# Kernel tuning notes

Measured on AMD Instinct MI355X. Metric: run time of the kernel, lower is better.

## Reference

```python
import jax, jax.numpy as jnp
import numpy as np

B, N, FIN, FOUT, H, U = 2, 2048, 128, 128, 4, 1024
ALPHA = 0.2  # LeakyReLU negative slope
NEG = -9e15  # mask value from the original code


def setup_inputs() -> dict:
    key = jax.random.key(0)
    k0, k1, k2, k3, k4 = jax.random.split(key, 5)
    x = jax.random.normal(k0, (B, N, FIN), dtype=jnp.float32)
    adj = jax.random.randint(k1, (B, N, N), 0, 2, dtype=jnp.int32)
    weights = jax.random.uniform(k2, (B, N - U, U), dtype=jnp.float32)
    # learned params, one per head (xavier-ish scaled normals)
    W = jax.random.normal(k3, (H, FIN, FOUT), dtype=jnp.float32) * 0.05
    a = jax.random.normal(k4, (H, 2 * FOUT, 1), dtype=jnp.float32) * 0.1
    return {"x": x, "weights": weights, "W": W, "a": a, "adj": adj}


def _build_bipartite_weights(weights, n):
    # weights: [B, v, u] -> dense [B, N, N] as in the original cat ops
    b, v, u = weights.shape
    wv = weights[:, :v, :]
    w1 = jnp.concatenate([jnp.zeros((b, u, u), weights.dtype), jnp.swapaxes(wv, 1, 2)], axis=2)  # [B,u,N]
    w2 = jnp.concatenate([wv, jnp.zeros((b, v, v), weights.dtype)], axis=2)                      # [B,v,N]
    return jnp.concatenate([w1, w2], axis=1)  # [B,N,N]


def reference(x, weights, W, a, adj):
    b, n, _ = x.shape
    big_w = _build_bipartite_weights(weights, n)  # [B,N,N]
    mask = adj > 0
    f = W.shape[2]
    outs = []
    for h in range(W.shape[0]):  # small fixed head count
        Wh = x @ W[h]  # [B,N,F]
        a_src = a[h, :f, 0]  # scores decompose: cat([Wh_i, Wh_j]) @ a == Wh_i@a_src + Wh_j@a_dst
        a_dst = a[h, f:, 0]
        e = jax.nn.leaky_relu((Wh @ a_src)[:, :, None] + (Wh @ a_dst)[:, None, :], negative_slope=ALPHA)  # [B,N,N]
        att = jnp.exp(jnp.where(mask, e, NEG)) * big_w
        denom = jnp.clip(jnp.sum(jnp.abs(att), axis=1, keepdims=True), 1e-12, None)  # F.normalize(p=1, dim=1)
        att = att / denom
        outs.append(jax.nn.elu(att @ Wh))  # concat=True head
    return jnp.concatenate(outs, axis=-1)  # [B,N,H*F]
```

## Files before the change

kernel.cpp:

```cpp
#include <hip/hip_runtime.h>
#include <hip/hip_bf16.h>
#include <math.h>

#define BB 2
#define NN 2048
#define FF 128
#define HH 4
#define HALF 1024

typedef __attribute__((ext_vector_type(8))) short short8;
typedef __attribute__((ext_vector_type(4))) short short4v;
typedef __attribute__((ext_vector_type(4))) float f32x4;

__device__ __forceinline__ short f2bf(float f){
    __hip_bfloat16 h = __float2bfloat16(f);
    return *reinterpret_cast<short*>(&h);
}
__device__ __forceinline__ float bf2f(short v){
    __hip_bfloat16 h = *reinterpret_cast<__hip_bfloat16*>(&v);
    return __bfloat162float(h);
}

__global__ __launch_bounds__(256) void k_whmm(const float* __restrict__ x,
        const float* __restrict__ W, const float* __restrict__ a,
        float* __restrict__ Wh, float* __restrict__ sT, float* __restrict__ dT,
        float* __restrict__ denom){
    __shared__ short xs[64 * 136];
    __shared__ short ws_[128 * 130];
    __shared__ float red_s[2][64], red_d[2][64];
    int t = threadIdx.x;
    int w = t >> 6, lane = t & 63;
    int wm = w >> 1, wn = w & 1;
    int n0 = blockIdx.x * 64;
    int h = blockIdx.y, b = blockIdx.z;
    int flat = blockIdx.x + 32 * (blockIdx.y + HH * blockIdx.z);
    if(t < 64) denom[flat * 64 + t] = 0.f;
    const float* xb = x + ((size_t)b * NN + n0) * FF;
    #pragma unroll
    for(int l = 0; l < 8; l++){
        int flat4 = t + l * 256;
        int row = flat4 >> 5, col4 = flat4 & 31;
        float4 v = *(const float4*)(xb + (size_t)row * FF + col4 * 4);
        short* dst = &xs[row * 136 + col4 * 4];
        dst[0] = f2bf(v.x); dst[1] = f2bf(v.y); dst[2] = f2bf(v.z); dst[3] = f2bf(v.w);
    }
    const float* Wb = W + (size_t)h * FF * FF;
    #pragma unroll
    for(int l = 0; l < 16; l++){
        int flat4 = t + l * 256;
        int row = flat4 >> 5, col4 = flat4 & 31;
        float4 v = *(const float4*)(Wb + (size_t)row * FF + col4 * 4);
        short* dst = &ws_[row * 130 + col4 * 4];
        dst[0] = f2bf(v.x); dst[1] = f2bf(v.y); dst[2] = f2bf(v.z); dst[3] = f2bf(v.w);
    }
    __syncthreads();
    int m = lane & 15, q = lane >> 4;
    f32x4 acc[2][4] = {};
    #pragma unroll
    for(int ks = 0; ks < 4; ks++){
        short8 af[2];
        #pragma unroll
        for(int mi = 0; mi < 2; mi++)
            af[mi] = *(const short8*)&xs[(wm * 32 + mi * 16 + m) * 136 + ks * 32 + q * 8];
        short8 bf[4];
        #pragma unroll
        for(int ni = 0; ni < 4; ni++){
            #pragma unroll
            for(int e = 0; e < 8; e++)
                bf[ni][e] = ws_[(ks * 32 + q * 8 + e) * 130 + wn * 64 + ni * 16 + m];
        }
        #pragma unroll
        for(int mi = 0; mi < 2; mi++)
            #pragma unroll
            for(int ni = 0; ni < 4; ni++)
                acc[mi][ni] = __builtin_amdgcn_mfma_f32_16x16x32_bf16(af[mi], bf[ni], acc[mi][ni], 0, 0, 0);
    }
    float* ob = Wh + (((size_t)b * HH + h) * NN + n0) * FF;
    #pragma unroll
    for(int mi = 0; mi < 2; mi++){
        #pragma unroll
        for(int ni = 0; ni < 4; ni++){
            int col = wn * 64 + ni * 16 + m;
            #pragma unroll
            for(int rg = 0; rg < 4; rg++){
                int row = wm * 32 + mi * 16 + q * 4 + rg;
                ob[(size_t)row * FF + col] = acc[mi][ni][rg];
            }
        }
    }
    float asrc[4], adst[4];
    const float* ah = a + (size_t)h * 2 * FF;
    #pragma unroll
    for(int ni = 0; ni < 4; ni++){
        int col = wn * 64 + ni * 16 + m;
        asrc[ni] = ah[col];
        adst[ni] = ah[FF + col];
    }
    #pragma unroll
    for(int mi = 0; mi < 2; mi++){
        #pragma unroll
        for(int rg = 0; rg < 4; rg++){
            float ps = 0.f, pd = 0.f;
            #pragma unroll
            for(int ni = 0; ni < 4; ni++){
                ps += acc[mi][ni][rg] * asrc[ni];
                pd += acc[mi][ni][rg] * adst[ni];
            }
            #pragma unroll
            for(int msk = 8; msk >= 1; msk >>= 1){
                ps += __shfl_xor(ps, msk);
                pd += __shfl_xor(pd, msk);
            }
            if(m == 0){
                int row = wm * 32 + mi * 16 + q * 4 + rg;
                red_s[wn][row] = ps;
                red_d[wn][row] = pd;
            }
        }
    }
    __syncthreads();
    if(t < 64){
        int n = n0 + t;
        sT[((size_t)b * NN + n) * HH + h] = red_s[0][t] + red_s[1][t];
        dT[((size_t)b * NN + n) * HH + h] = red_d[0][t] + red_d[1][t];
    }
}

__global__ __launch_bounds__(256) void k_att(const int* __restrict__ adj,
        const float* __restrict__ wv,
        const float* __restrict__ sT, const float* __restrict__ dT,
        short* __restrict__ P, float* __restrict__ denom){
    __shared__ float red[HH][128];
    int t = threadIdx.x;
    int jlane = t & 127, ihalf = t >> 7;
    int jt = blockIdx.x, ic = blockIdx.y, bb = blockIdx.z;
    int b = bb >> 1, blk = bb & 1;
    int jl = jt * 128 + jlane;
    int jg = blk ? jl : HALF + jl;
    int iloc0 = ic * 32 + ihalf * 16;
    int ig0 = (blk ? HALF : 0) + iloc0;
    const int* ap = adj + ((size_t)b * NN + ig0) * NN + jg;
    const float* sp = sT + ((size_t)b * NN + ig0) * HH;
    float4 dv4 = *(const float4*)(dT + ((size_t)b * NN + jg) * HH);
    float da[4] = {dv4.x, dv4.y, dv4.z, dv4.w};
    short* Pp = P + ((size_t)(bb * HH) << 20) + (size_t)iloc0 * 1024 + jl;
    float den[HH] = {};
#define ATTLOOP(WPTR, WSTRIDE) \
    _Pragma("unroll 4") \
    for(int ii = 0; ii < 16; ii++){ \
        int av = ap[(size_t)ii * NN]; \
        float wq = (WPTR)[(size_t)ii * (WSTRIDE)]; \
        float4 s4 = *(const float4*)(sp + ii * HH); \
        float wmv = av > 0 ? wq : 0.f; \
        float sa[4] = {s4.x, s4.y, s4.z, s4.w}; \
        _Pragma("unroll") \
        for(int h = 0; h < HH; h++){ \
            float tt = sa[h] + da[h]; \
            tt = tt > 0.f ? tt : 0.2f * tt; \
            float pe = __expf(tt) * wmv; \
            den[h] += pe; \
            Pp[((size_t)h << 20) + (size_t)ii * 1024] = f2bf(pe); \
        } \
    }
    if(blk){
        const float* wp = wv + ((size_t)b * HALF + iloc0) * HALF + jl;
        ATTLOOP(wp, HALF)
    } else {
        const float* wp = wv + ((size_t)b * HALF + jl) * HALF + iloc0;
        ATTLOOP(wp, 1)
    }
#undef ATTLOOP
    if(ihalf){
        #pragma unroll
        for(int h = 0; h < HH; h++) red[h][jlane] = den[h];
    }
    __syncthreads();
    if(!ihalf){
        #pragma unroll
        for(int h = 0; h < HH; h++)
            atomicAdd(&denom[((size_t)b * HH + h) * NN + jg], den[h] + red[h][jlane]);
    }
}

__global__ __launch_bounds__(256) void k_scale(const float* __restrict__ Wh,
        const float* __restrict__ denom, short* __restrict__ WhB){
    int t = threadIdx.x, w = t >> 6, lane = t & 63, q = lane >> 4, r = lane & 15;
    int kt = blockIdx.x, h = blockIdx.y, b = blockIdx.z;
    int sl = b * HH + h;
    int jb = kt * 32 + q * 8;
    const float* dp = denom + (size_t)sl * NN + jb;
    float4 D0 = *(const float4*)dp;
    float4 D1 = *(const float4*)(dp + 4);
    float dn[8] = {D0.x,D0.y,D0.z,D0.w,D1.x,D1.y,D1.z,D1.w};
    float inv[8];
    #pragma unroll
    for(int e = 0; e < 8; e++) inv[e] = 1.f / fmaxf(dn[e], 1e-12f);
    #pragma unroll
    for(int ntl = 0; ntl < 2; ntl++){
        int nt = w + ntl * 4;
        int f = nt * 16 + r;
        short8 pk;
        #pragma unroll
        for(int e = 0; e < 8; e++){
            float v = Wh[((size_t)sl * NN + jb + e) * FF + f] * inv[e];
            pk[e] = f2bf(v);
        }
        *(short8*)(WhB + (((size_t)sl * 8 + nt) * 64 + kt) * 512 + lane * 8) = pk;
    }
}

__global__ __launch_bounds__(256) void k_pv(const short* __restrict__ P,
        const short* __restrict__ WhB, float* __restrict__ out){
    __shared__ short lds[2][6656];
    int t = threadIdx.x;
    int w = t >> 6, lane = t & 63;
    int wm = w >> 1, wn = w & 1;
    int mt = blockIdx.x, h = blockIdx.y, bb = blockIdx.z;
    int b = bb >> 1, blk = bb & 1;
    const short* Prow = P + ((size_t)(bb * HH + h) << 20);
    size_t Bb2 = ((size_t)b * HH + h) * 8;
    int koff = blk ? 0 : 32;
    int rowA = t >> 3, c8 = t & 7;
    const short* srcA0 = Prow + (size_t)(mt * 32 + rowA) * 1024 + c8 * 4;
    f32x4 acc[4] = {};
    short4v r0; short8 r1, r2;
#define LOADST(KT) { \
    r0 = *(const short4v*)(srcA0 + (KT) * 32); \
    r1 = *(const short8*)(WhB + ((Bb2 + (t >> 6)) * 64 + koff + (KT)) * 512 + (t & 63) * 8); \
    r2 = *(const short8*)(WhB + ((Bb2 + 4 + (t >> 6)) * 64 + koff + (KT)) * 512 + (t & 63) * 8); }
#define WRITEST(BUF) { \
    *(short4v*)&lds[BUF][rowA * 40 + c8 * 4] = r0; \
    *(short8*)&lds[BUF][2560 + (t >> 6) * 512 + (t & 63) * 8] = r1; \
    *(short8*)&lds[BUF][2560 + 2048 + (t >> 6) * 512 + (t & 63) * 8] = r2; }
    LOADST(0)
    WRITEST(0)
    __syncthreads();
    int m = lane & 15, q = lane >> 4;
    for(int kt = 0; kt < 32; kt++){
        int cur = kt & 1;
        if(kt < 31){ LOADST(kt + 1) }
        short8 af = *(const short8*)&lds[cur][(wm * 16 + m) * 40 + q * 8];
        short8 bf[4];
        #pragma unroll
        for(int ni = 0; ni < 4; ni++)
            bf[ni] = *(const short8*)&lds[cur][2560 + (wn * 4 + ni) * 512 + lane * 8];
        #pragma unroll
        for(int ni = 0; ni < 4; ni++)
            acc[ni] = __builtin_amdgcn_mfma_f32_16x16x32_bf16(af, bf[ni], acc[ni], 0, 0, 0);
        __syncthreads();
        if(kt < 31){
            WRITEST(cur ^ 1)
            __syncthreads();
        }
    }
    int rq = lane >> 4, rc = lane & 15;
    int rowg0 = (blk ? HALF : 0) + mt * 32 + wm * 16;
    #pragma unroll
    for(int ni = 0; ni < 4; ni++){
        int f = (wn * 4 + ni) * 16 + rc;
        #pragma unroll
        for(int rg = 0; rg < 4; rg++){
            float v = acc[ni][rg];
            v = v > 0.f ? v : expm1f(v);
            out[((size_t)b * NN + rowg0 + rq * 4 + rg) * (HH * FF) + h * FF + f] = v;
        }
    }
#undef LOADST
#undef WRITEST
}

extern "C" void kernel_launch(void* const* d_in, const int* in_sizes, int n_in,
                              void* d_out, int out_size, void* d_ws, size_t ws_size,
                              hipStream_t stream){
    const float* x   = (const float*)d_in[0];
    const float* wv  = (const float*)d_in[1];
    const float* W   = (const float*)d_in[2];
    const float* a   = (const float*)d_in[3];
    const int*   adj = (const int*)d_in[4];
    float* out = (float*)d_out;

    char* ws = (char*)d_ws;
    short* P     = (short*)ws;
    float* Wh    = (float*)(ws + 33554432);
    short* WhB   = (short*)(ws + 41943040);
    float* sT    = (float*)(ws + 46137344);
    float* dT    = (float*)(ws + 46202880);
    float* denom = (float*)(ws + 46268416);

    k_whmm<<<dim3(32, HH, BB), 256, 0, stream>>>(x, W, a, Wh, sT, dT, denom);
    k_att<<<dim3(8, 32, 4), 256, 0, stream>>>(adj, wv, sT, dT, P, denom);
    k_scale<<<dim3(64, HH, BB), 256, 0, stream>>>(Wh, denom, WhB);
    k_pv<<<dim3(32, HH, 4), 256, 0, stream>>>(P, WhB, out);
}
```

Measured before the change: 48.34 us.

## Fuse attention recompute into PV matmul, drop materialized P matrix

```diff
diff --git a/kernel.cpp b/kernel.cpp
--- a/kernel.cpp
+++ b/kernel.cpp
@@ -9,7 +9,7 @@
 #define HALF 1024
 
 typedef __attribute__((ext_vector_type(8))) short short8;
-typedef __attribute__((ext_vector_type(4))) short short4v;
+typedef __attribute__((ext_vector_type(16))) short short16;
 typedef __attribute__((ext_vector_type(4))) float f32x4;
 
 __device__ __forceinline__ short f2bf(float f){
@@ -21,9 +21,33 @@
     return __bfloat162float(h);
 }
 
+__global__ void k_wvt(const float* __restrict__ wv, __hip_bfloat16* __restrict__ wvT,
+                      __hip_bfloat16* __restrict__ wvB){
+    __shared__ float tile[32][33];
+    int b = blockIdx.z;
+    int i0 = blockIdx.x * 32, j0 = blockIdx.y * 32;
+    int tx = threadIdx.x & 31, ty = threadIdx.x >> 5;
+    const float* src = wv + (size_t)b * HALF * HALF;
+    __hip_bfloat16* dstT = wvT + (size_t)b * HALF * HALF;
+    __hip_bfloat16* dstB = wvB + (size_t)b * HALF * HALF;
+    #pragma unroll
+    for(int l = 0; l < 4; l++){
+        int row = ty + l * 8;
+        float v = src[(size_t)(j0 + row) * HALF + (i0 + tx)];
+        tile[row][tx] = v;
+        dstB[(size_t)(j0 + row) * HALF + (i0 + tx)] = __float2bfloat16(v);
+    }
+    __syncthreads();
+    #pragma unroll
+    for(int l = 0; l < 4; l++){
+        int row = ty + l * 8;
+        dstT[(size_t)(i0 + row) * HALF + (j0 + tx)] = __float2bfloat16(tile[tx][row]);
+    }
+}
+
 __global__ __launch_bounds__(256) void k_whmm(const float* __restrict__ x,
         const float* __restrict__ W, const float* __restrict__ a,
-        float* __restrict__ Wh, float* __restrict__ sT, float* __restrict__ dT,
+        short* __restrict__ WhB, float* __restrict__ sT, float* __restrict__ dT,
         float* __restrict__ denom){
     __shared__ short xs[64 * 136];
     __shared__ short ws_[128 * 130];
@@ -33,6 +57,7 @@
     int wm = w >> 1, wn = w & 1;
     int n0 = blockIdx.x * 64;
     int h = blockIdx.y, b = blockIdx.z;
+    int sl = b * HH + h;
     int flat = blockIdx.x + 32 * (blockIdx.y + HH * blockIdx.z);
     if(t < 64) denom[flat * 64 + t] = 0.f;
     const float* xb = x + ((size_t)b * NN + n0) * FF;
@@ -74,19 +99,6 @@
             #pragma unroll
             for(int ni = 0; ni < 4; ni++)
                 acc[mi][ni] = __builtin_amdgcn_mfma_f32_16x16x32_bf16(af[mi], bf[ni], acc[mi][ni], 0, 0, 0);
-    }
-    float* ob = Wh + (((size_t)b * HH + h) * NN + n0) * FF;
-    #pragma unroll
-    for(int mi = 0; mi < 2; mi++){
-        #pragma unroll
-        for(int ni = 0; ni < 4; ni++){
-            int col = wn * 64 + ni * 16 + m;
-            #pragma unroll
-            for(int rg = 0; rg < 4; rg++){
-                int row = wm * 32 + mi * 16 + q * 4 + rg;
-                ob[(size_t)row * FF + col] = acc[mi][ni][rg];
-            }
-        }
     }
     float asrc[4], adst[4];
     const float* ah = a + (size_t)h * 2 * FF;
@@ -119,17 +131,41 @@
         }
     }
     __syncthreads();
+    short* cs = xs;
+    #pragma unroll
+    for(int mi = 0; mi < 2; mi++){
+        #pragma unroll
+        for(int ni = 0; ni < 4; ni++){
+            int col = wn * 64 + ni * 16 + m;
+            #pragma unroll
+            for(int rg = 0; rg < 4; rg++){
+                int row = wm * 32 + mi * 16 + q * 4 + rg;
+                cs[row * 130 + col] = f2bf(acc[mi][ni][rg]);
+            }
+        }
+    }
     if(t < 64){
         int n = n0 + t;
         sT[((size_t)b * NN + n) * HH + h] = red_s[0][t] + red_s[1][t];
         dT[((size_t)b * NN + n) * HH + h] = red_d[0][t] + red_d[1][t];
     }
-}
-
-__global__ __launch_bounds__(256) void k_att(const int* __restrict__ adj,
-        const float* __restrict__ wv,
+    __syncthreads();
+    #pragma unroll
+    for(int fi = 0; fi < 4; fi++){
+        int fragId = w * 4 + fi;
+        int ktg = fragId >> 3, nt = fragId & 7;
+        short8 pk;
+        #pragma unroll
+        for(int e = 0; e < 8; e++)
+            pk[e] = cs[(ktg * 32 + q * 8 + e) * 130 + nt * 16 + m];
+        *(short8*)(WhB + (((size_t)sl * 8 + nt) * 64 + blockIdx.x * 2 + ktg) * 512 + lane * 8) = pk;
+    }
+}
+
+__global__ __launch_bounds__(256) void k_denom(const int* __restrict__ adj,
+        const __hip_bfloat16* __restrict__ wvB, const __hip_bfloat16* __restrict__ wvT,
         const float* __restrict__ sT, const float* __restrict__ dT,
-        short* __restrict__ P, float* __restrict__ denom){
+        float* __restrict__ denom){
     __shared__ float red[HH][128];
     int t = threadIdx.x;
     int jlane = t & 127, ihalf = t >> 7;
@@ -140,36 +176,25 @@
     int iloc0 = ic * 32 + ihalf * 16;
     int ig0 = (blk ? HALF : 0) + iloc0;
     const int* ap = adj + ((size_t)b * NN + ig0) * NN + jg;
+    const short* wp = (const short*)(blk ? wvB : wvT) + ((size_t)b * HALF + iloc0) * HALF + jl;
     const float* sp = sT + ((size_t)b * NN + ig0) * HH;
     float4 dv4 = *(const float4*)(dT + ((size_t)b * NN + jg) * HH);
     float da[4] = {dv4.x, dv4.y, dv4.z, dv4.w};
-    short* Pp = P + ((size_t)(bb * HH) << 20) + (size_t)iloc0 * 1024 + jl;
     float den[HH] = {};
-#define ATTLOOP(WPTR, WSTRIDE) \
-    _Pragma("unroll 4") \
-    for(int ii = 0; ii < 16; ii++){ \
-        int av = ap[(size_t)ii * NN]; \
-        float wq = (WPTR)[(size_t)ii * (WSTRIDE)]; \
-        float4 s4 = *(const float4*)(sp + ii * HH); \
-        float wmv = av > 0 ? wq : 0.f; \
-        float sa[4] = {s4.x, s4.y, s4.z, s4.w}; \
-        _Pragma("unroll") \
-        for(int h = 0; h < HH; h++){ \
-            float tt = sa[h] + da[h]; \
-            tt = tt > 0.f ? tt : 0.2f * tt; \
-            float pe = __expf(tt) * wmv; \
-            den[h] += pe; \
-            Pp[((size_t)h << 20) + (size_t)ii * 1024] = f2bf(pe); \
-        } \
-    }
-    if(blk){
-        const float* wp = wv + ((size_t)b * HALF + iloc0) * HALF + jl;
-        ATTLOOP(wp, HALF)
-    } else {
-        const float* wp = wv + ((size_t)b * HALF + jl) * HALF + iloc0;
-        ATTLOOP(wp, 1)
-    }
-#undef ATTLOOP
+    #pragma unroll 4
+    for(int ii = 0; ii < 16; ii++){
+        int av = ap[(size_t)ii * NN];
+        short wq = wp[(size_t)ii * HALF];
+        float4 s4 = *(const float4*)(sp + ii * HH);
+        float wmv = av > 0 ? bf2f(wq) : 0.f;
+        float sa[4] = {s4.x, s4.y, s4.z, s4.w};
+        #pragma unroll
+        for(int h = 0; h < HH; h++){
+            float tt = sa[h] + da[h];
+            tt = tt > 0.f ? tt : 0.2f * tt;
+            den[h] += __expf(tt) * wmv;
+        }
+    }
     if(ihalf){
         #pragma unroll
         for(int h = 0; h < HH; h++) red[h][jlane] = den[h];
@@ -182,91 +207,88 @@
     }
 }
 
-__global__ __launch_bounds__(256) void k_scale(const float* __restrict__ Wh,
-        const float* __restrict__ denom, short* __restrict__ WhB){
-    int t = threadIdx.x, w = t >> 6, lane = t & 63, q = lane >> 4, r = lane & 15;
-    int kt = blockIdx.x, h = blockIdx.y, b = blockIdx.z;
-    int sl = b * HH + h;
-    int jb = kt * 32 + q * 8;
-    const float* dp = denom + (size_t)sl * NN + jb;
-    float4 D0 = *(const float4*)dp;
-    float4 D1 = *(const float4*)(dp + 4);
-    float dn[8] = {D0.x,D0.y,D0.z,D0.w,D1.x,D1.y,D1.z,D1.w};
-    float inv[8];
-    #pragma unroll
-    for(int e = 0; e < 8; e++) inv[e] = 1.f / fmaxf(dn[e], 1e-12f);
-    #pragma unroll
-    for(int ntl = 0; ntl < 2; ntl++){
-        int nt = w + ntl * 4;
-        int f = nt * 16 + r;
-        short8 pk;
-        #pragma unroll
-        for(int e = 0; e < 8; e++){
-            float v = Wh[((size_t)sl * NN + jb + e) * FF + f] * inv[e];
-            pk[e] = f2bf(v);
-        }
-        *(short8*)(WhB + (((size_t)sl * 8 + nt) * 64 + kt) * 512 + lane * 8) = pk;
-    }
-}
-
-__global__ __launch_bounds__(256) void k_pv(const short* __restrict__ P,
-        const short* __restrict__ WhB, float* __restrict__ out){
-    __shared__ short lds[2][6656];
+__global__ __launch_bounds__(512) void k_attpv(const int* __restrict__ adj,
+        const __hip_bfloat16* __restrict__ wvB, const __hip_bfloat16* __restrict__ wvT,
+        const float* __restrict__ sT, const float* __restrict__ dT,
+        const float* __restrict__ denom, const short* __restrict__ WhB,
+        float* __restrict__ out){
+    __shared__ short Ps[64 * 72];
+    __shared__ short Bs[16 * 512];
     int t = threadIdx.x;
     int w = t >> 6, lane = t & 63;
     int wm = w >> 1, wn = w & 1;
     int mt = blockIdx.x, h = blockIdx.y, bb = blockIdx.z;
     int b = bb >> 1, blk = bb & 1;
-    const short* Prow = P + ((size_t)(bb * HH + h) << 20);
-    size_t Bb2 = ((size_t)b * HH + h) * 8;
+    int sl = b * HH + h;
+    int iloc0 = mt * 64;
+    int igb = (blk ? HALF : 0) + iloc0;
+    int col0 = blk ? 0 : HALF;
     int koff = blk ? 0 : 32;
-    int rowA = t >> 3, c8 = t & 7;
-    const short* srcA0 = Prow + (size_t)(mt * 32 + rowA) * 1024 + c8 * 4;
+    int iA = t >> 3, jj = t & 7, j8 = jj * 8;
+    const int* apb = adj + ((size_t)b * NN + igb + iA) * NN + col0;
+    const short* wpb = (const short*)(blk ? wvB : wvT) + ((size_t)b * HALF + iloc0 + iA) * HALF;
+    const float* dpb = dT + ((size_t)b * NN + col0) * HH + h;
+    const float* npb = denom + (size_t)sl * NN + col0;
+    float sA = sT[((size_t)b * NN + igb + iA) * HH + h];
+    int fragI = t >> 5;
+    int ktf = fragI >> 3, ntf = fragI & 7;
+    int ln2 = (t & 31) * 2;
+    const short* Bsrc = WhB + (((size_t)sl * 8 + ntf) * 64 + koff + ktf) * 512 + ln2 * 8;
+    int4 A0, A1; short8 WQ; short16 BV;
+    float dA[8], nA[8];
+#define LOADT(JT) { \
+    A0 = *(const int4*)(apb + (size_t)(JT) * 64 + j8); \
+    A1 = *(const int4*)(apb + (size_t)(JT) * 64 + j8 + 4); \
+    WQ = *(const short8*)(wpb + (JT) * 64 + j8); \
+    _Pragma("unroll") \
+    for(int e_ = 0; e_ < 8; e_++) dA[e_] = dpb[((JT) * 64 + j8 + e_) * HH]; \
+    float4 n0_ = *(const float4*)(npb + (JT) * 64 + j8); \
+    float4 n1_ = *(const float4*)(npb + (JT) * 64 + j8 + 4); \
+    nA[0]=n0_.x; nA[1]=n0_.y; nA[2]=n0_.z; nA[3]=n0_.w; \
+    nA[4]=n1_.x; nA[5]=n1_.y; nA[6]=n1_.z; nA[7]=n1_.w; \
+    BV = *(const short16*)(Bsrc + (size_t)(JT) * 1024); }
     f32x4 acc[4] = {};
-    short4v r0; short8 r1, r2;
-#define LOADST(KT) { \
-    r0 = *(const short4v*)(srcA0 + (KT) * 32); \
-    r1 = *(const short8*)(WhB + ((Bb2 + (t >> 6)) * 64 + koff + (KT)) * 512 + (t & 63) * 8); \
-    r2 = *(const short8*)(WhB + ((Bb2 + 4 + (t >> 6)) * 64 + koff + (KT)) * 512 + (t & 63) * 8); }
-#define WRITEST(BUF) { \
-    *(short4v*)&lds[BUF][rowA * 40 + c8 * 4] = r0; \
-    *(short8*)&lds[BUF][2560 + (t >> 6) * 512 + (t & 63) * 8] = r1; \
-    *(short8*)&lds[BUF][2560 + 2048 + (t >> 6) * 512 + (t & 63) * 8] = r2; }
-    LOADST(0)
-    WRITEST(0)
-    __syncthreads();
-    int m = lane & 15, q = lane >> 4;
-    for(int kt = 0; kt < 32; kt++){
-        int cur = kt & 1;
-        if(kt < 31){ LOADST(kt + 1) }
-        short8 af = *(const short8*)&lds[cur][(wm * 16 + m) * 40 + q * 8];
-        short8 bf[4];
-        #pragma unroll
-        for(int ni = 0; ni < 4; ni++)
-            bf[ni] = *(const short8*)&lds[cur][2560 + (wn * 4 + ni) * 512 + lane * 8];
-        #pragma unroll
-        for(int ni = 0; ni < 4; ni++)
-            acc[ni] = __builtin_amdgcn_mfma_f32_16x16x32_bf16(af, bf[ni], acc[ni], 0, 0, 0);
+    LOADT(0)
+    for(int jt = 0; jt < 16; jt++){
+        int aa[8] = {A0.x, A0.y, A0.z, A0.w, A1.x, A1.y, A1.z, A1.w};
+        short8 pk;
+        #pragma unroll
+        for(int e = 0; e < 8; e++){
+            float wmv = aa[e] > 0 ? bf2f(WQ[e]) : 0.f;
+            float inv = 1.f / fmaxf(nA[e], 1e-12f);
+            float tt = sA + dA[e];
+            tt = tt > 0.f ? tt : 0.2f * tt;
+            pk[e] = f2bf(__expf(tt) * wmv * inv);
+        }
         __syncthreads();
-        if(kt < 31){
-            WRITEST(cur ^ 1)
-            __syncthreads();
-        }
-    }
-    int rq = lane >> 4, rc = lane & 15;
-    int rowg0 = (blk ? HALF : 0) + mt * 32 + wm * 16;
+        *(short8*)&Ps[iA * 72 + j8] = pk;
+        *(short16*)&Bs[fragI * 512 + ln2 * 8] = BV;
+        if(jt < 15){ LOADT(jt + 1) }
+        __syncthreads();
+        int m = lane & 15, q = lane >> 4;
+        short8 af0 = *(const short8*)&Ps[(wm * 16 + m) * 72 + q * 8];
+        short8 af1 = *(const short8*)&Ps[(wm * 16 + m) * 72 + 32 + q * 8];
+        #pragma unroll
+        for(int ni = 0; ni < 4; ni++){
+            short8 bf0 = *(const short8*)&Bs[((wn * 4 + ni) * 64 + lane) * 8];
+            short8 bf1 = *(const short8*)&Bs[((8 + wn * 4 + ni) * 64 + lane) * 8];
+            acc[ni] = __builtin_amdgcn_mfma_f32_16x16x32_bf16(af0, bf0, acc[ni], 0, 0, 0);
+            acc[ni] = __builtin_amdgcn_mfma_f32_16x16x32_bf16(af1, bf1, acc[ni], 0, 0, 0);
+        }
+    }
+#undef LOADT
+    int q = lane >> 4, rc = lane & 15;
     #pragma unroll
     for(int ni = 0; ni < 4; ni++){
-        int f = (wn * 4 + ni) * 16 + rc;
+        int f = wn * 64 + ni * 16 + rc;
         #pragma unroll
         for(int rg = 0; rg < 4; rg++){
+            int grow = igb + wm * 16 + q * 4 + rg;
             float v = acc[ni][rg];
             v = v > 0.f ? v : expm1f(v);
-            out[((size_t)b * NN + rowg0 + rq * 4 + rg) * (HH * FF) + h * FF + f] = v;
-        }
-    }
-#undef LOADST
-#undef WRITEST
+            out[((size_t)b * NN + grow) * (HH * FF) + h * FF + f] = v;
+        }
+    }
 }
 
 extern "C" void kernel_launch(void* const* d_in, const int* in_sizes, int n_in,
@@ -280,15 +302,15 @@
     float* out = (float*)d_out;
 
     char* ws = (char*)d_ws;
-    short* P     = (short*)ws;
-    float* Wh    = (float*)(ws + 33554432);
-    short* WhB   = (short*)(ws + 41943040);
-    float* sT    = (float*)(ws + 46137344);
-    float* dT    = (float*)(ws + 46202880);
-    float* denom = (float*)(ws + 46268416);
-
-    k_whmm<<<dim3(32, HH, BB), 256, 0, stream>>>(x, W, a, Wh, sT, dT, denom);
-    k_att<<<dim3(8, 32, 4), 256, 0, stream>>>(adj, wv, sT, dT, P, denom);
-    k_scale<<<dim3(64, HH, BB), 256, 0, stream>>>(Wh, denom, WhB);
-    k_pv<<<dim3(32, HH, 4), 256, 0, stream>>>(P, WhB, out);
-}
+    short*          WhB   = (short*)ws;
+    __hip_bfloat16* wvT   = (__hip_bfloat16*)(ws + 4194304);
+    __hip_bfloat16* wvB   = (__hip_bfloat16*)(ws + 8388608);
+    float*          sT    = (float*)(ws + 12582912);
+    float*          dT    = (float*)(ws + 12648448);
+    float*          denom = (float*)(ws + 12713984);
+
+    k_wvt<<<dim3(32, 32, BB), 256, 0, stream>>>(wv, wvT, wvB);
+    k_whmm<<<dim3(32, HH, BB), 256, 0, stream>>>(x, W, a, WhB, sT, dT, denom);
+    k_denom<<<dim3(8, 32, 4), 256, 0, stream>>>(adj, wvB, wvT, sT, dT, denom);
+    k_attpv<<<dim3(16, HH, 4), 512, 0, stream>>>(adj, wvB, wvT, sT, dT, denom, WhB, out);
+}
```

Result: slower. 61.50 us (+27.2%).

## Fuse Wh packing into projection kernel and apply column normalization in PV load

Applied to the files above, without the earlier changes.

```diff
diff --git a/kernel.cpp b/kernel.cpp
--- a/kernel.cpp
+++ b/kernel.cpp
@@ -23,7 +23,7 @@
 
 __global__ __launch_bounds__(256) void k_whmm(const float* __restrict__ x,
         const float* __restrict__ W, const float* __restrict__ a,
-        float* __restrict__ Wh, float* __restrict__ sT, float* __restrict__ dT,
+        short* __restrict__ WhB, float* __restrict__ sT, float* __restrict__ dT,
         float* __restrict__ denom){
     __shared__ short xs[64 * 136];
     __shared__ short ws_[128 * 130];
@@ -33,6 +33,7 @@
     int wm = w >> 1, wn = w & 1;
     int n0 = blockIdx.x * 64;
     int h = blockIdx.y, b = blockIdx.z;
+    int sl = b * HH + h;
     int flat = blockIdx.x + 32 * (blockIdx.y + HH * blockIdx.z);
     if(t < 64) denom[flat * 64 + t] = 0.f;
     const float* xb = x + ((size_t)b * NN + n0) * FF;
@@ -75,19 +76,6 @@
             for(int ni = 0; ni < 4; ni++)
                 acc[mi][ni] = __builtin_amdgcn_mfma_f32_16x16x32_bf16(af[mi], bf[ni], acc[mi][ni], 0, 0, 0);
     }
-    float* ob = Wh + (((size_t)b * HH + h) * NN + n0) * FF;
-    #pragma unroll
-    for(int mi = 0; mi < 2; mi++){
-        #pragma unroll
-        for(int ni = 0; ni < 4; ni++){
-            int col = wn * 64 + ni * 16 + m;
-            #pragma unroll
-            for(int rg = 0; rg < 4; rg++){
-                int row = wm * 32 + mi * 16 + q * 4 + rg;
-                ob[(size_t)row * FF + col] = acc[mi][ni][rg];
-            }
-        }
-    }
     float asrc[4], adst[4];
     const float* ah = a + (size_t)h * 2 * FF;
     #pragma unroll
@@ -119,10 +107,34 @@
         }
     }
     __syncthreads();
+    short* cs = xs;
+    #pragma unroll
+    for(int mi = 0; mi < 2; mi++){
+        #pragma unroll
+        for(int ni = 0; ni < 4; ni++){
+            int col = wn * 64 + ni * 16 + m;
+            #pragma unroll
+            for(int rg = 0; rg < 4; rg++){
+                int row = wm * 32 + mi * 16 + q * 4 + rg;
+                cs[row * 130 + col] = f2bf(acc[mi][ni][rg]);
+            }
+        }
+    }
     if(t < 64){
         int n = n0 + t;
         sT[((size_t)b * NN + n) * HH + h] = red_s[0][t] + red_s[1][t];
         dT[((size_t)b * NN + n) * HH + h] = red_d[0][t] + red_d[1][t];
+    }
+    __syncthreads();
+    #pragma unroll
+    for(int fi = 0; fi < 4; fi++){
+        int fragId = w * 4 + fi;
+        int ktg = fragId >> 3, nt = fragId & 7;
+        short8 pk;
+        #pragma unroll
+        for(int e = 0; e < 8; e++)
+            pk[e] = cs[(ktg * 32 + q * 8 + e) * 130 + nt * 16 + m];
+        *(short8*)(WhB + (((size_t)sl * 8 + nt) * 64 + blockIdx.x * 2 + ktg) * 512 + lane * 8) = pk;
     }
 }
 
@@ -182,54 +194,37 @@
     }
 }
 
-__global__ __launch_bounds__(256) void k_scale(const float* __restrict__ Wh,
-        const float* __restrict__ denom, short* __restrict__ WhB){
-    int t = threadIdx.x, w = t >> 6, lane = t & 63, q = lane >> 4, r = lane & 15;
-    int kt = blockIdx.x, h = blockIdx.y, b = blockIdx.z;
-    int sl = b * HH + h;
-    int jb = kt * 32 + q * 8;
-    const float* dp = denom + (size_t)sl * NN + jb;
-    float4 D0 = *(const float4*)dp;
-    float4 D1 = *(const float4*)(dp + 4);
-    float dn[8] = {D0.x,D0.y,D0.z,D0.w,D1.x,D1.y,D1.z,D1.w};
-    float inv[8];
-    #pragma unroll
-    for(int e = 0; e < 8; e++) inv[e] = 1.f / fmaxf(dn[e], 1e-12f);
-    #pragma unroll
-    for(int ntl = 0; ntl < 2; ntl++){
-        int nt = w + ntl * 4;
-        int f = nt * 16 + r;
-        short8 pk;
-        #pragma unroll
-        for(int e = 0; e < 8; e++){
-            float v = Wh[((size_t)sl * NN + jb + e) * FF + f] * inv[e];
-            pk[e] = f2bf(v);
-        }
-        *(short8*)(WhB + (((size_t)sl * 8 + nt) * 64 + kt) * 512 + lane * 8) = pk;
-    }
-}
-
 __global__ __launch_bounds__(256) void k_pv(const short* __restrict__ P,
-        const short* __restrict__ WhB, float* __restrict__ out){
+        const float* __restrict__ denom, const short* __restrict__ WhB,
+        float* __restrict__ out){
     __shared__ short lds[2][6656];
     int t = threadIdx.x;
     int w = t >> 6, lane = t & 63;
     int wm = w >> 1, wn = w & 1;
     int mt = blockIdx.x, h = blockIdx.y, bb = blockIdx.z;
     int b = bb >> 1, blk = bb & 1;
+    int sl = b * HH + h;
     const short* Prow = P + ((size_t)(bb * HH + h) << 20);
-    size_t Bb2 = ((size_t)b * HH + h) * 8;
+    size_t Bb2 = ((size_t)sl) * 8;
     int koff = blk ? 0 : 32;
+    int col0 = blk ? 0 : HALF;
+    const float* npb = denom + (size_t)sl * NN + col0;
     int rowA = t >> 3, c8 = t & 7;
     const short* srcA0 = Prow + (size_t)(mt * 32 + rowA) * 1024 + c8 * 4;
     f32x4 acc[4] = {};
-    short4v r0; short8 r1, r2;
+    short4v r0; short8 r1, r2; float4 n4;
 #define LOADST(KT) { \
     r0 = *(const short4v*)(srcA0 + (KT) * 32); \
+    n4 = *(const float4*)(npb + (KT) * 32 + c8 * 4); \
     r1 = *(const short8*)(WhB + ((Bb2 + (t >> 6)) * 64 + koff + (KT)) * 512 + (t & 63) * 8); \
     r2 = *(const short8*)(WhB + ((Bb2 + 4 + (t >> 6)) * 64 + koff + (KT)) * 512 + (t & 63) * 8); }
 #define WRITEST(BUF) { \
-    *(short4v*)&lds[BUF][rowA * 40 + c8 * 4] = r0; \
+    short4v rs_; \
+    rs_[0] = f2bf(bf2f(r0[0]) * __builtin_amdgcn_rcpf(fmaxf(n4.x, 1e-12f))); \
+    rs_[1] = f2bf(bf2f(r0[1]) * __builtin_amdgcn_rcpf(fmaxf(n4.y, 1e-12f))); \
+    rs_[2] = f2bf(bf2f(r0[2]) * __builtin_amdgcn_rcpf(fmaxf(n4.z, 1e-12f))); \
+    rs_[3] = f2bf(bf2f(r0[3]) * __builtin_amdgcn_rcpf(fmaxf(n4.w, 1e-12f))); \
+    *(short4v*)&lds[BUF][rowA * 40 + c8 * 4] = rs_; \
     *(short8*)&lds[BUF][2560 + (t >> 6) * 512 + (t & 63) * 8] = r1; \
     *(short8*)&lds[BUF][2560 + 2048 + (t >> 6) * 512 + (t & 63) * 8] = r2; }
     LOADST(0)
@@ -281,14 +276,12 @@
 
     char* ws = (char*)d_ws;
     short* P     = (short*)ws;
-    float* Wh    = (float*)(ws + 33554432);
-    short* WhB   = (short*)(ws + 41943040);
-    float* sT    = (float*)(ws + 46137344);
-    float* dT    = (float*)(ws + 46202880);
-    float* denom = (float*)(ws + 46268416);
-
-    k_whmm<<<dim3(32, HH, BB), 256, 0, stream>>>(x, W, a, Wh, sT, dT, denom);
+    short* WhB   = (short*)(ws + 33554432);
+    float* sT    = (float*)(ws + 37748736);
+    float* dT    = (float*)(ws + 37814272);
+    float* denom = (float*)(ws + 37879808);
+
+    k_whmm<<<dim3(32, HH, BB), 256, 0, stream>>>(x, W, a, WhB, sT, dT, denom);
     k_att<<<dim3(8, 32, 4), 256, 0, stream>>>(adj, wv, sT, dT, P, denom);
-    k_scale<<<dim3(64, HH, BB), 256, 0, stream>>>(Wh, denom, WhB);
-    k_pv<<<dim3(32, HH, 4), 256, 0, stream>>>(P, WhB, out);
-}
+    k_pv<<<dim3(32, HH, 4), 256, 0, stream>>>(P, denom, WhB, out);
+}
```

Result: no change. 47.90 us (-0.9%).
